# Performance work log

Measured on AMD Instinct MI355X. Metric: run time of the kernel, lower is better.

The kernel has to match this reference:

```python
import jax, jax.numpy as jnp
import numpy as np

N = 50000
E = 1600000
VOCAB = 1000
EMB = 128
HID = 128
OUT = 128


def setup_inputs() -> dict:
    key = jax.random.key(0)
    ks = jax.random.split(key, 8)
    labels = jax.random.randint(ks[0], (N,), 0, VOCAB)
    edge_index = jax.random.randint(ks[1], (2, E), 0, N)
    weight = jax.random.uniform(ks[2], (E,), dtype=jnp.float32)
    emb_table = jax.random.normal(ks[3], (VOCAB, EMB), dtype=jnp.float32) * 0.02
    W1 = jax.random.normal(ks[4], (EMB, HID), dtype=jnp.float32) * (1.0 / np.sqrt(EMB))
    b1 = jnp.zeros((HID,), dtype=jnp.float32)
    W2 = jax.random.normal(ks[5], (HID, OUT), dtype=jnp.float32) * (1.0 / np.sqrt(HID))
    b2 = jnp.zeros((OUT,), dtype=jnp.float32)
    return {"labels": labels, "edge_index": edge_index, "weight": weight,
            "emb_table": emb_table, "W1": W1, "b1": b1, "W2": W2, "b2": b2}


def _gcn_conv(x, src, dst, ew, W, b, n_nodes):
    # PyG GCNConv: linear transform, then symmetric-normalized weighted aggregation.
    x = x @ W  # [N, F_out]
    deg = jax.ops.segment_sum(ew, dst, num_segments=n_nodes)  # weighted in-degree (incl. self loops)
    dinv = jnp.where(deg > 0, jax.lax.rsqrt(deg), 0.0)
    norm = dinv[src] * ew * dinv[dst]  # [E_tot]
    msg = x[src] * norm[:, None]  # gather + scale
    out = jax.ops.segment_sum(msg, dst, num_segments=n_nodes)  # scatter-add
    return out + b


def reference(labels, edge_index, weight, emb_table, W1, b1, W2, b2):
    n_nodes = emb_table.shape[0] if False else labels.shape[0]
    # add self loops with weight 1.0 (GCNConv default add_self_loops=True)
    loop = jnp.arange(n_nodes, dtype=edge_index.dtype)
    src = jnp.concatenate([edge_index[0], loop])
    dst = jnp.concatenate([edge_index[1], loop])
    ew = jnp.concatenate([weight.astype(jnp.float32), jnp.ones((n_nodes,), jnp.float32)])

    x = emb_table[labels]  # embedding lookup [N, EMB]
    x = _gcn_conv(x, src, dst, ew, W1, b1, n_nodes)
    x = jax.nn.relu(x)
    x = _gcn_conv(x, src, dst, ew, W2, b2, n_nodes)
    return x
```

## Files before the change

kernel.cpp:

```cpp
#include <hip/hip_runtime.h>
#include <hip/hip_fp16.h>


#define CHUNKS 256
#define BSTAGE 2816

typedef float floatx2 __attribute__((ext_vector_type(2)));

__global__ __launch_bounds__(1024) void hist_temb_kernel(
    const int* __restrict__ dst, int* __restrict__ hist, int e, int chunk,
    int nb, int bact, const float* __restrict__ emb,
    const float* __restrict__ W1, __half* __restrict__ temb, int vocab) {
  __shared__ unsigned lh[1024];
  __shared__ float xs[8][128];
  int b = blockIdx.x, t = threadIdx.x;
  if (b < bact) {
    lh[t] = 0;
    __syncthreads();
    int start = b * chunk, end = min(e, start + chunk);
    for (int i = start + t; i < end; i += 1024) atomicAdd(&lh[dst[i] >> 6], 1u);
    __syncthreads();
    if (t < nb) hist[(size_t)t * CHUNKS + b] = (int)lh[t];
  } else {
    int r = (b - bact) * 8 + (t >> 7);
    int j = t & 127;
    if (r < vocab) xs[t >> 7][j] = emb[r * 128 + j];
    __syncthreads();
    if (r < vocab) {
      float acc = 0.f;
#pragma unroll 8
      for (int k = 0; k < 128; ++k) acc = fmaf(xs[t >> 7][k], W1[k * 128 + j], acc);
      temb[r * 128 + j] = __float2half_rn(acc);
    }
  }
}

__global__ __launch_bounds__(256) void colscan_kernel(const int* __restrict__ hist,
                                                      int* __restrict__ off,
                                                      int* __restrict__ tot,
                                                      int nb, int bact) {
  int k = (blockIdx.x * 256 + threadIdx.x) >> 6;
  int lane = threadIdx.x & 63;
  if (k >= nb) return;
  int carry = 0;
  for (int r = 0; r < CHUNKS / 64; ++r) {
    int b = r * 64 + lane;
    int h = (b < bact) ? hist[(size_t)k * CHUNKS + b] : 0;
    int x = h;
#pragma unroll
    for (int d = 1; d < 64; d <<= 1) {
      int tt = __shfl_up(x, d, 64);
      if (lane >= d) x += tt;
    }
    if (b < bact) off[(size_t)k * CHUNKS + b] = carry + x - h;
    carry += __shfl(x, 63, 64);
  }
  if (lane == 0) tot[k] = carry;
}

__global__ __launch_bounds__(1024) void ebase_kernel(const int* __restrict__ tot,
                                                     int* __restrict__ ebase, int nb) {
  __shared__ int wsum[16];
  int t = threadIdx.x, lane = t & 63, wv = t >> 6;
  int v = (t < nb) ? tot[t] : 0;
  int x = v;
#pragma unroll
  for (int d = 1; d < 64; d <<= 1) {
    int tt = __shfl_up(x, d, 64);
    if (lane >= d) x += tt;
  }
  if (lane == 63) wsum[wv] = x;
  __syncthreads();
  int o = 0;
#pragma unroll
  for (int w = 0; w < 16; ++w) o += (w < wv) ? wsum[w] : 0;
  int excl = x - v + o;
  if (t < nb) ebase[t] = excl;
  if (t == nb - 1) ebase[nb] = excl + v;
}

__global__ __launch_bounds__(1024) void scatter_kernel(
    const int* __restrict__ src, const int* __restrict__ dst,
    const float* __restrict__ w, const int* __restrict__ labels,
    const int* __restrict__ off, const int* __restrict__ ebase,
    int2* __restrict__ brec, int e, int chunk, int nb) {
  __shared__ unsigned bincnt[1024];
  __shared__ int gbase[1024];
  int b = blockIdx.x, t = threadIdx.x;
  bincnt[t] = 0;
  if (t < nb) gbase[t] = ebase[t] + off[(size_t)t * CHUNKS + b];
  __syncthreads();
  int start = b * chunk, end = min(e, start + chunk);
  int s[7], d[7], lb[7], ps[7];
  float wv[7];
#pragma unroll
  for (int u = 0; u < 7; ++u) {
    int i = start + u * 1024 + t;
    bool ok = i < end;
    s[u] = ok ? src[i] : 0;
    d[u] = ok ? dst[i] : 0;
    wv[u] = ok ? w[i] : 0.f;
  }
#pragma unroll
  for (int u = 0; u < 7; ++u) lb[u] = labels[s[u]];
#pragma unroll
  for (int u = 0; u < 7; ++u) ps[u] = gbase[d[u] >> 6];
#pragma unroll
  for (int u = 0; u < 7; ++u) {
    int i = start + u * 1024 + t;
    if (i < end) {
      int k = d[u] >> 6;
      unsigned lr = atomicAdd(&bincnt[k], 1u);
      unsigned rx = (unsigned)s[u] | ((unsigned)(d[u] & 63) << 16) |
                    ((unsigned)lb[u] << 22);
      brec[ps[u] + (int)lr] = make_int2((int)rx, __float_as_int(wv[u]));
    }
  }
}

__global__ __launch_bounds__(256) void bsort_kernel(const int2* __restrict__ brec,
                                                    const int* __restrict__ ebase,
                                                    int2* __restrict__ csr,
                                                    int* __restrict__ rs,
                                                    float* __restrict__ dinv, int n) {
  __shared__ int2 stage[BSTAGE];
  __shared__ unsigned h64[2][64];
  __shared__ unsigned cur[2][64];
  __shared__ float rsum[2][64];
  int k = blockIdx.x, t = threadIdx.x;
  int p = t >> 7;
  int e0 = ebase[k], e1 = ebase[k + 1], cnt = e1 - e0;
  if (t < 128) { h64[t >> 6][t & 63] = 0; rsum[t >> 6][t & 63] = 0.f; }
  __syncthreads();
  bool fits = (cnt <= BSTAGE);
  for (int i = t; i < cnt; i += 256) {
    int2 r = brec[e0 + i];
    if (fits) stage[i] = r;
    unsigned dl = ((unsigned)r.x >> 16) & 63u;
    atomicAdd(&h64[p][dl], 1u);
    atomicAdd(&rsum[p][dl], __int_as_float(r.y));
  }
  __syncthreads();
  if (t < 64) {
    int h0 = (int)h64[0][t];
    int hv = h0 + (int)h64[1][t];
    int x = hv;
#pragma unroll
    for (int d = 1; d < 64; d <<= 1) {
      int tt = __shfl_up(x, d, 64);
      if (t >= d) x += tt;
    }
    int ex = x - hv;
    cur[0][t] = (unsigned)(e0 + ex);
    cur[1][t] = (unsigned)(e0 + ex + h0);
    int v = k * 64 + t;
    if (v <= n) rs[v] = e0 + ex;
    if (v < n) dinv[v] = rsqrtf(1.0f + rsum[0][t] + rsum[1][t]);
  }
  __syncthreads();
  for (int i = t; i < cnt; i += 256) {
    int2 r = fits ? stage[i] : brec[e0 + i];
    unsigned rx = (unsigned)r.x;
    int dl = (int)((rx >> 16) & 63u);
    int pos = (int)atomicAdd(&cur[p][dl], 1u);
    csr[pos] = make_int2((int)((rx & 0xffffu) | ((rx >> 22) << 16)), r.y);
  }
}

__device__ __forceinline__ void unpack4(float2 raw, float2& a, float2& b) {
  union { float f; __half2 h; } u0, u1;
  u0.f = raw.x;
  u1.f = raw.y;
  a = __half22float2(u0.h);
  b = __half22float2(u1.h);
}

__global__ __launch_bounds__(256) void agg1_kernel(
    const int* __restrict__ rs, const int2* __restrict__ csr,
    const float* __restrict__ dinv, const int* __restrict__ labels,
    const __half* __restrict__ temb, const float* __restrict__ b1,
    unsigned* __restrict__ out8, int n) {
  int wid = (blockIdx.x * blockDim.x + threadIdx.x) >> 6;
  int lane = threadIdx.x & 63;
  if (wid >= n) return;
  int half = lane >> 5, fl = lane & 31;
  unsigned flo = (unsigned)(fl << 3);
  const char* tb = (const char*)temb;
  float di = dinv[wid];
  float acc0, acc1, acc2, acc3;
  {
    unsigned off = ((unsigned)labels[wid] << 8) + flo;
    float2 raw = *(const float2*)(tb + off);
    float2 a, b;
    unpack4(raw, a, b);
    float ss = half ? 0.f : di;
    acc0 = a.x * ss; acc1 = a.y * ss; acc2 = b.x * ss; acc3 = b.y * ss;
  }
  int base0 = rs[wid], r1v = rs[wid + 1];
  int s = 0;
  float v = 0.f;
  if (base0 + lane < r1v) {
    int2 c = csr[base0 + lane];
    s = c.x;
    v = __int_as_float(c.y) * dinv[c.x & 0xffff];
  }
  for (int base = base0; base < r1v; base += 64) {
    int ns = 0;
    float nv = 0.f;
    if (base + 64 + lane < r1v) {
      int2 c = csr[base + 64 + lane];
      ns = c.x;
      nv = __int_as_float(c.y) * dinv[c.x & 0xffff];
    }
    int nb = min(64, r1v - base);
    int j = 0;
    for (; j + 16 <= nb; j += 16) {
#pragma unroll
      for (int u = 0; u < 8; ++u) {
        int jj = j + 2 * u + half;
        int sj = __shfl(s, jj, 64);
        float vj = __shfl(v, jj, 64);
        unsigned off = (((unsigned)sj >> 16) << 8) + flo;
        float2 raw = *(const float2*)(tb + off);
        float2 a, b;
        unpack4(raw, a, b);
        acc0 = fmaf(a.x, vj, acc0); acc1 = fmaf(a.y, vj, acc1);
        acc2 = fmaf(b.x, vj, acc2); acc3 = fmaf(b.y, vj, acc3);
      }
    }
    for (; j + 2 <= nb; j += 2) {
      int jj = j + half;
      int sj = __shfl(s, jj, 64);
      float vj = __shfl(v, jj, 64);
      unsigned off = (((unsigned)sj >> 16) << 8) + flo;
      float2 raw = *(const float2*)(tb + off);
      float2 a, b;
      unpack4(raw, a, b);
      acc0 = fmaf(a.x, vj, acc0); acc1 = fmaf(a.y, vj, acc1);
      acc2 = fmaf(b.x, vj, acc2); acc3 = fmaf(b.y, vj, acc3);
    }
    if (j < nb) {
      int sj = __shfl(s, j, 64);
      float vj0 = __shfl(v, j, 64);
      float vj = half ? 0.f : vj0;
      unsigned off = (((unsigned)sj >> 16) << 8) + flo;
      float2 raw = *(const float2*)(tb + off);
      float2 a, b;
      unpack4(raw, a, b);
      acc0 = fmaf(a.x, vj, acc0); acc1 = fmaf(a.y, vj, acc1);
      acc2 = fmaf(b.x, vj, acc2); acc3 = fmaf(b.y, vj, acc3);
    }
    s = ns;
    v = nv;
  }
  acc0 += __shfl_xor(acc0, 32, 64);
  acc1 += __shfl_xor(acc1, 32, 64);
  acc2 += __shfl_xor(acc2, 32, 64);
  acc3 += __shfl_xor(acc3, 32, 64);
  if (half == 0) {
    float4 b4 = ((const float4*)b1)[fl];
    acc0 = fmaxf(fmaf(acc0, di, b4.x), 0.f) * 64.f;
    acc1 = fmaxf(fmaf(acc1, di, b4.y), 0.f) * 64.f;
    acc2 = fmaxf(fmaf(acc2, di, b4.z), 0.f) * 64.f;
    acc3 = fmaxf(fmaf(acc3, di, b4.w), 0.f) * 64.f;
    int pk = __builtin_amdgcn_cvt_pk_fp8_f32(acc0, acc1, 0, false);
    pk = __builtin_amdgcn_cvt_pk_fp8_f32(acc2, acc3, pk, true);
    out8[(size_t)wid * 32 + fl] = (unsigned)pk;
  }
}

__global__ __launch_bounds__(256) void agg2_kernel(
    const int* __restrict__ rs, const int2* __restrict__ csr,
    const float* __restrict__ dinv, const unsigned* __restrict__ h8,
    float* __restrict__ out, int n) {
  int wid = (blockIdx.x * blockDim.x + threadIdx.x) >> 6;
  int lane = threadIdx.x & 63;
  if (wid >= n) return;
  int half = lane >> 5, fl = lane & 31;
  unsigned flo = (unsigned)(fl << 2);
  const char* hb = (const char*)h8;
  float di = dinv[wid];
  float acc0, acc1, acc2, acc3;
  {
    unsigned r8 = *(const unsigned*)(hb + ((unsigned)wid << 7) + flo);
    floatx2 a = __builtin_amdgcn_cvt_pk_f32_fp8((int)r8, false);
    floatx2 b = __builtin_amdgcn_cvt_pk_f32_fp8((int)r8, true);
    float ss = half ? 0.f : di;
    acc0 = a[0] * ss; acc1 = a[1] * ss; acc2 = b[0] * ss; acc3 = b[1] * ss;
  }
  int base0 = rs[wid], r1v = rs[wid + 1];
  int s = 0;
  float v = 0.f;
  if (base0 + lane < r1v) {
    int2 c = csr[base0 + lane];
    s = c.x;
    v = __int_as_float(c.y) * dinv[c.x & 0xffff];
  }
  for (int base = base0; base < r1v; base += 64) {
    int ns = 0;
    float nv = 0.f;
    if (base + 64 + lane < r1v) {
      int2 c = csr[base + 64 + lane];
      ns = c.x;
      nv = __int_as_float(c.y) * dinv[c.x & 0xffff];
    }
    int nb = min(64, r1v - base);
    int j = 0;
    for (; j + 16 <= nb; j += 16) {
#pragma unroll
      for (int u = 0; u < 8; ++u) {
        int jj = j + 2 * u + half;
        int sj = __shfl(s, jj, 64);
        float vj = __shfl(v, jj, 64);
        unsigned off = (((unsigned)sj & 0xffffu) << 7) + flo;
        unsigned r8 = *(const unsigned*)(hb + off);
        floatx2 a = __builtin_amdgcn_cvt_pk_f32_fp8((int)r8, false);
        floatx2 b = __builtin_amdgcn_cvt_pk_f32_fp8((int)r8, true);
        acc0 = fmaf(a[0], vj, acc0); acc1 = fmaf(a[1], vj, acc1);
        acc2 = fmaf(b[0], vj, acc2); acc3 = fmaf(b[1], vj, acc3);
      }
    }
    for (; j + 2 <= nb; j += 2) {
      int jj = j + half;
      int sj = __shfl(s, jj, 64);
      float vj = __shfl(v, jj, 64);
      unsigned off = (((unsigned)sj & 0xffffu) << 7) + flo;
      unsigned r8 = *(const unsigned*)(hb + off);
      floatx2 a = __builtin_amdgcn_cvt_pk_f32_fp8((int)r8, false);
      floatx2 b = __builtin_amdgcn_cvt_pk_f32_fp8((int)r8, true);
      acc0 = fmaf(a[0], vj, acc0); acc1 = fmaf(a[1], vj, acc1);
      acc2 = fmaf(b[0], vj, acc2); acc3 = fmaf(b[1], vj, acc3);
    }
    if (j < nb) {
      int sj = __shfl(s, j, 64);
      float vj0 = __shfl(v, j, 64);
      float vj = half ? 0.f : vj0;
      unsigned off = (((unsigned)sj & 0xffffu) << 7) + flo;
      unsigned r8 = *(const unsigned*)(hb + off);
      floatx2 a = __builtin_amdgcn_cvt_pk_f32_fp8((int)r8, false);
      floatx2 b = __builtin_amdgcn_cvt_pk_f32_fp8((int)r8, true);
      acc0 = fmaf(a[0], vj, acc0); acc1 = fmaf(a[1], vj, acc1);
      acc2 = fmaf(b[0], vj, acc2); acc3 = fmaf(b[1], vj, acc3);
    }
    s = ns;
    v = nv;
  }
  acc0 += __shfl_xor(acc0, 32, 64);
  acc1 += __shfl_xor(acc1, 32, 64);
  acc2 += __shfl_xor(acc2, 32, 64);
  acc3 += __shfl_xor(acc3, 32, 64);
  if (half == 0) {
    float sc = di * 0.015625f;
    ((float4*)(out + (size_t)wid * 128))[fl] =
        make_float4(acc0 * sc, acc1 * sc, acc2 * sc, acc3 * sc);
  }
}

__global__ __launch_bounds__(256) void gemm_bias_kernel(float* __restrict__ y,
                                                        const float* __restrict__ W,
                                                        const float* __restrict__ bias,
                                                        int n) {
  __shared__ float xs[32][128];
  int tid = threadIdx.x;
  int tc = tid & 31;
  int tr = tid >> 5;
  int rb = blockIdx.x * 32;
  {
    const float4* xg = (const float4*)(y + (size_t)rb * 128);
    float4* xls = (float4*)&xs[0][0];
#pragma unroll
    for (int i = 0; i < 4; ++i) {
      int idx = tid + i * 256;
      int row = rb + (idx >> 5);
      float4 val = (row < n) ? xg[idx] : make_float4(0.f, 0.f, 0.f, 0.f);
      xls[idx] = val;
    }
  }
  __syncthreads();
  int j0 = tc * 4;
  float4 b4 = *(const float4*)(bias + j0);
  float acc[4][4];
#pragma unroll
  for (int r = 0; r < 4; ++r) {
    acc[r][0] = b4.x; acc[r][1] = b4.y; acc[r][2] = b4.z; acc[r][3] = b4.w;
  }
#pragma unroll 4
  for (int k = 0; k < 128; ++k) {
    float4 w4 = *(const float4*)(W + k * 128 + j0);
#pragma unroll
    for (int r = 0; r < 4; ++r) {
      float xv = xs[tr * 4 + r][k];
      acc[r][0] = fmaf(xv, w4.x, acc[r][0]);
      acc[r][1] = fmaf(xv, w4.y, acc[r][1]);
      acc[r][2] = fmaf(xv, w4.z, acc[r][2]);
      acc[r][3] = fmaf(xv, w4.w, acc[r][3]);
    }
  }
#pragma unroll
  for (int r = 0; r < 4; ++r) {
    int row = rb + tr * 4 + r;
    if (row < n)
      *(float4*)(y + (size_t)row * 128 + j0) =
          make_float4(acc[r][0], acc[r][1], acc[r][2], acc[r][3]);
  }
}

extern "C" void kernel_launch(void* const* d_in, const int* in_sizes, int n_in,
                              void* d_out, int out_size, void* d_ws, size_t ws_size,
                              hipStream_t stream) {
  const int* labels = (const int*)d_in[0];
  const int* edge_index = (const int*)d_in[1];
  const float* weight = (const float*)d_in[2];
  const float* emb = (const float*)d_in[3];
  const float* W1 = (const float*)d_in[4];
  const float* b1 = (const float*)d_in[5];
  const float* W2 = (const float*)d_in[6];
  const float* b2 = (const float*)d_in[7];

  int n = in_sizes[0];
  int e = in_sizes[1] / 2;
  int vocab = in_sizes[3] / 128;
  const int* srcp = edge_index;
  const int* dstp = edge_index + e;

  int nb = (n + 63) >> 6;
  int chunk = (e + CHUNKS - 1) / CHUNKS;
  int bact = (e + chunk - 1) / chunk;
  int tblocks = (vocab + 7) / 8;

  float* ws = (float*)d_ws;
  size_t o = 0;
  auto alloc_f = [&](size_t c) { float* p = ws + o; o += (c + 255) & ~(size_t)255; return p; };
  int*      hist  = (int*)alloc_f((size_t)nb * CHUNKS);
  int*      off   = (int*)alloc_f((size_t)nb * CHUNKS);
  int*      tot   = (int*)alloc_f(nb);
  int*      ebase = (int*)alloc_f(nb + 1);
  int2*     brec  = (int2*)alloc_f((size_t)e * 2);
  int*      rs    = (int*)alloc_f(n + 1);
  int2*     csr   = (int2*)alloc_f((size_t)e * 2);
  float*    dinv  = alloc_f(n);
  __half*   temb  = (__half*)alloc_f((size_t)vocab * 64);
  unsigned* out8  = (unsigned*)alloc_f((size_t)n * 32);
  (void)ws_size;

  dim3 b256(256);
  dim3 b1024(1024);
  int gagg = (int)(((size_t)n * 64 + 255) / 256);

  hist_temb_kernel<<<bact + tblocks, b1024, 0, stream>>>(dstp, hist, e, chunk, nb,
                                                         bact, emb, W1, temb, vocab);
  colscan_kernel<<<(nb * 64 + 255) / 256, b256, 0, stream>>>(hist, off, tot, nb, bact);
  ebase_kernel<<<1, b1024, 0, stream>>>(tot, ebase, nb);
  scatter_kernel<<<bact, b1024, 0, stream>>>(srcp, dstp, weight, labels, off, ebase,
                                             brec, e, chunk, nb);
  bsort_kernel<<<nb, b256, 0, stream>>>(brec, ebase, csr, rs, dinv, n);
  agg1_kernel<<<gagg, b256, 0, stream>>>(rs, csr, dinv, labels, temb, b1, out8, n);
  agg2_kernel<<<gagg, b256, 0, stream>>>(rs, csr, dinv, out8, (float*)d_out, n);
  gemm_bias_kernel<<<(n + 31) / 32, b256, 0, stream>>>((float*)d_out, W2, b2, n);
}
```

Baseline: 165.6 us.

## Repack CSR to 4-byte records with prescaled fp16 weights and store temb in fp8

Adds a repack kernel that turns each 8-byte CSR record into two 4-byte arrays, one per aggregation pass. Each packs the needed source index (label or node id) with an fp16 edge weight already multiplied by dinv[src]. The aggregation kernels therefore no longer do a per-edge dinv gather, and the streamed edge data is halved. The embedding-times-W1 table is now stored in fp8 scaled by 64 instead of fp16, which shrinks gathered rows, and that GEMM uses float4 loads with 32 rows per block. The cost is an extra kernel pass over all edges and lower precision in both the edge weights and the first-layer features.

```diff
diff --git a/kernel.cpp b/kernel.cpp
--- a/kernel.cpp
+++ b/kernel.cpp
@@ -10,9 +10,9 @@
 __global__ __launch_bounds__(1024) void hist_temb_kernel(
     const int* __restrict__ dst, int* __restrict__ hist, int e, int chunk,
     int nb, int bact, const float* __restrict__ emb,
-    const float* __restrict__ W1, __half* __restrict__ temb, int vocab) {
+    const float* __restrict__ W1, unsigned* __restrict__ temb8, int vocab) {
   __shared__ unsigned lh[1024];
-  __shared__ float xs[8][128];
+  __shared__ float xs[32][128];
   int b = blockIdx.x, t = threadIdx.x;
   if (b < bact) {
     lh[t] = 0;
@@ -22,15 +22,23 @@
     __syncthreads();
     if (t < nb) hist[(size_t)t * CHUNKS + b] = (int)lh[t];
   } else {
-    int r = (b - bact) * 8 + (t >> 7);
-    int j = t & 127;
-    if (r < vocab) xs[t >> 7][j] = emb[r * 128 + j];
+    int row = t >> 5, fl = t & 31;
+    int r = (b - bact) * 32 + row;
+    if (r < vocab)
+      *(float4*)&xs[row][fl * 4] = *(const float4*)(emb + (size_t)r * 128 + fl * 4);
     __syncthreads();
     if (r < vocab) {
-      float acc = 0.f;
-#pragma unroll 8
-      for (int k = 0; k < 128; ++k) acc = fmaf(xs[t >> 7][k], W1[k * 128 + j], acc);
-      temb[r * 128 + j] = __float2half_rn(acc);
+      float a0 = 0.f, a1 = 0.f, a2 = 0.f, a3 = 0.f;
+#pragma unroll 4
+      for (int k = 0; k < 128; ++k) {
+        float xv = xs[row][k];
+        float4 w4 = *(const float4*)(W1 + k * 128 + fl * 4);
+        a0 = fmaf(xv, w4.x, a0); a1 = fmaf(xv, w4.y, a1);
+        a2 = fmaf(xv, w4.z, a2); a3 = fmaf(xv, w4.w, a3);
+      }
+      int pk = __builtin_amdgcn_cvt_pk_fp8_f32(a0 * 64.f, a1 * 64.f, 0, false);
+      pk = __builtin_amdgcn_cvt_pk_fp8_f32(a2 * 64.f, a3 * 64.f, pk, true);
+      temb8[(size_t)r * 32 + fl] = (unsigned)pk;
     }
   }
 }
@@ -167,91 +175,93 @@
   }
 }
 
-__device__ __forceinline__ void unpack4(float2 raw, float2& a, float2& b) {
-  union { float f; __half2 h; } u0, u1;
-  u0.f = raw.x;
-  u1.f = raw.y;
-  a = __half22float2(u0.h);
-  b = __half22float2(u1.h);
+__global__ __launch_bounds__(256) void repack_kernel(const int2* __restrict__ csr,
+                                                     const float* __restrict__ dinv,
+                                                     unsigned* __restrict__ csrA,
+                                                     unsigned* __restrict__ csrB,
+                                                     int e) {
+  int i = blockIdx.x * 1024 + threadIdx.x;
+  int2 c[4];
+  float wp[4];
+#pragma unroll
+  for (int u = 0; u < 4; ++u) {
+    int k = i + u * 256;
+    c[u] = (k < e) ? csr[k] : make_int2(0, 0);
+  }
+#pragma unroll
+  for (int u = 0; u < 4; ++u)
+    wp[u] = __int_as_float(c[u].y) * dinv[c[u].x & 0xffff];
+#pragma unroll
+  for (int u = 0; u < 4; ++u) {
+    int k = i + u * 256;
+    if (k < e) {
+      unsigned hb = (unsigned)__half_as_ushort(__float2half_rn(wp[u]));
+      csrA[k] = ((((unsigned)c[u].x) >> 16) << 16) | hb;
+      csrB[k] = (((unsigned)c[u].x) << 16) | hb;
+    }
+  }
 }
 
 __global__ __launch_bounds__(256) void agg1_kernel(
-    const int* __restrict__ rs, const int2* __restrict__ csr,
+    const int* __restrict__ rs, const unsigned* __restrict__ csrA,
     const float* __restrict__ dinv, const int* __restrict__ labels,
-    const __half* __restrict__ temb, const float* __restrict__ b1,
+    const unsigned* __restrict__ temb8, const float* __restrict__ b1,
     unsigned* __restrict__ out8, int n) {
   int wid = (blockIdx.x * blockDim.x + threadIdx.x) >> 6;
   int lane = threadIdx.x & 63;
   if (wid >= n) return;
   int half = lane >> 5, fl = lane & 31;
-  unsigned flo = (unsigned)(fl << 3);
-  const char* tb = (const char*)temb;
+  unsigned flo = (unsigned)(fl << 2);
+  const char* tb = (const char*)temb8;
   float di = dinv[wid];
   float acc0, acc1, acc2, acc3;
   {
-    unsigned off = ((unsigned)labels[wid] << 8) + flo;
-    float2 raw = *(const float2*)(tb + off);
-    float2 a, b;
-    unpack4(raw, a, b);
+    unsigned r8 = *(const unsigned*)(tb + (((unsigned)labels[wid]) << 7) + flo);
+    floatx2 a = __builtin_amdgcn_cvt_pk_f32_fp8((int)r8, false);
+    floatx2 b = __builtin_amdgcn_cvt_pk_f32_fp8((int)r8, true);
     float ss = half ? 0.f : di;
-    acc0 = a.x * ss; acc1 = a.y * ss; acc2 = b.x * ss; acc3 = b.y * ss;
+    acc0 = a[0] * ss; acc1 = a[1] * ss; acc2 = b[0] * ss; acc3 = b[1] * ss;
   }
   int base0 = rs[wid], r1v = rs[wid + 1];
-  int s = 0;
-  float v = 0.f;
-  if (base0 + lane < r1v) {
-    int2 c = csr[base0 + lane];
-    s = c.x;
-    v = __int_as_float(c.y) * dinv[c.x & 0xffff];
-  }
+  unsigned x = 0;
+  if (base0 + lane < r1v) x = csrA[base0 + lane];
   for (int base = base0; base < r1v; base += 64) {
-    int ns = 0;
-    float nv = 0.f;
-    if (base + 64 + lane < r1v) {
-      int2 c = csr[base + 64 + lane];
-      ns = c.x;
-      nv = __int_as_float(c.y) * dinv[c.x & 0xffff];
-    }
+    unsigned nx = 0;
+    if (base + 64 + lane < r1v) nx = csrA[base + 64 + lane];
     int nb = min(64, r1v - base);
     int j = 0;
     for (; j + 16 <= nb; j += 16) {
 #pragma unroll
       for (int u = 0; u < 8; ++u) {
-        int jj = j + 2 * u + half;
-        int sj = __shfl(s, jj, 64);
-        float vj = __shfl(v, jj, 64);
-        unsigned off = (((unsigned)sj >> 16) << 8) + flo;
-        float2 raw = *(const float2*)(tb + off);
-        float2 a, b;
-        unpack4(raw, a, b);
-        acc0 = fmaf(a.x, vj, acc0); acc1 = fmaf(a.y, vj, acc1);
-        acc2 = fmaf(b.x, vj, acc2); acc3 = fmaf(b.y, vj, acc3);
+        unsigned xj = (unsigned)__shfl((int)x, j + 2 * u + half, 64);
+        float vj = __half2float(__ushort_as_half((unsigned short)(xj & 0xffffu)));
+        unsigned r8 = *(const unsigned*)(tb + ((xj >> 16) << 7) + flo);
+        floatx2 a = __builtin_amdgcn_cvt_pk_f32_fp8((int)r8, false);
+        floatx2 b = __builtin_amdgcn_cvt_pk_f32_fp8((int)r8, true);
+        acc0 = fmaf(a[0], vj, acc0); acc1 = fmaf(a[1], vj, acc1);
+        acc2 = fmaf(b[0], vj, acc2); acc3 = fmaf(b[1], vj, acc3);
       }
     }
     for (; j + 2 <= nb; j += 2) {
-      int jj = j + half;
-      int sj = __shfl(s, jj, 64);
-      float vj = __shfl(v, jj, 64);
-      unsigned off = (((unsigned)sj >> 16) << 8) + flo;
-      float2 raw = *(const float2*)(tb + off);
-      float2 a, b;
-      unpack4(raw, a, b);
-      acc0 = fmaf(a.x, vj, acc0); acc1 = fmaf(a.y, vj, acc1);
-      acc2 = fmaf(b.x, vj, acc2); acc3 = fmaf(b.y, vj, acc3);
+      unsigned xj = (unsigned)__shfl((int)x, j + half, 64);
+      float vj = __half2float(__ushort_as_half((unsigned short)(xj & 0xffffu)));
+      unsigned r8 = *(const unsigned*)(tb + ((xj >> 16) << 7) + flo);
+      floatx2 a = __builtin_amdgcn_cvt_pk_f32_fp8((int)r8, false);
+      floatx2 b = __builtin_amdgcn_cvt_pk_f32_fp8((int)r8, true);
+      acc0 = fmaf(a[0], vj, acc0); acc1 = fmaf(a[1], vj, acc1);
+      acc2 = fmaf(b[0], vj, acc2); acc3 = fmaf(b[1], vj, acc3);
     }
     if (j < nb) {
-      int sj = __shfl(s, j, 64);
-      float vj0 = __shfl(v, j, 64);
+      unsigned xj = (unsigned)__shfl((int)x, j, 64);
+      float vj0 = __half2float(__ushort_as_half((unsigned short)(xj & 0xffffu)));
       float vj = half ? 0.f : vj0;
-      unsigned off = (((unsigned)sj >> 16) << 8) + flo;
-      float2 raw = *(const float2*)(tb + off);
-      float2 a, b;
-      unpack4(raw, a, b);
-      acc0 = fmaf(a.x, vj, acc0); acc1 = fmaf(a.y, vj, acc1);
-      acc2 = fmaf(b.x, vj, acc2); acc3 = fmaf(b.y, vj, acc3);
-    }
-    s = ns;
-    v = nv;
+      unsigned r8 = *(const unsigned*)(tb + ((xj >> 16) << 7) + flo);
+      floatx2 a = __builtin_amdgcn_cvt_pk_f32_fp8((int)r8, false);
+      floatx2 b = __builtin_amdgcn_cvt_pk_f32_fp8((int)r8, true);
+      acc0 = fmaf(a[0], vj, acc0); acc1 = fmaf(a[1], vj, acc1);
+      acc2 = fmaf(b[0], vj, acc2); acc3 = fmaf(b[1], vj, acc3);
+    }
+    x = nx;
   }
   acc0 += __shfl_xor(acc0, 32, 64);
   acc1 += __shfl_xor(acc1, 32, 64);
@@ -259,10 +269,10 @@
   acc3 += __shfl_xor(acc3, 32, 64);
   if (half == 0) {
     float4 b4 = ((const float4*)b1)[fl];
-    acc0 = fmaxf(fmaf(acc0, di, b4.x), 0.f) * 64.f;
-    acc1 = fmaxf(fmaf(acc1, di, b4.y), 0.f) * 64.f;
-    acc2 = fmaxf(fmaf(acc2, di, b4.z), 0.f) * 64.f;
-    acc3 = fmaxf(fmaf(acc3, di, b4.w), 0.f) * 64.f;
+    acc0 = fmaxf(fmaf(acc0, di, b4.x * 64.f), 0.f);
+    acc1 = fmaxf(fmaf(acc1, di, b4.y * 64.f), 0.f);
+    acc2 = fmaxf(fmaf(acc2, di, b4.z * 64.f), 0.f);
+    acc3 = fmaxf(fmaf(acc3, di, b4.w * 64.f), 0.f);
     int pk = __builtin_amdgcn_cvt_pk_fp8_f32(acc0, acc1, 0, false);
     pk = __builtin_amdgcn_cvt_pk_fp8_f32(acc2, acc3, pk, true);
     out8[(size_t)wid * 32 + fl] = (unsigned)pk;
@@ -270,7 +280,7 @@
 }
 
 __global__ __launch_bounds__(256) void agg2_kernel(
-    const int* __restrict__ rs, const int2* __restrict__ csr,
+    const int* __restrict__ rs, const unsigned* __restrict__ csrB,
     const float* __restrict__ dinv, const unsigned* __restrict__ h8,
     float* __restrict__ out, int n) {
   int wid = (blockIdx.x * blockDim.x + threadIdx.x) >> 6;
@@ -282,38 +292,26 @@
   float di = dinv[wid];
   float acc0, acc1, acc2, acc3;
   {
-    unsigned r8 = *(const unsigned*)(hb + ((unsigned)wid << 7) + flo);
+    unsigned r8 = *(const unsigned*)(hb + (((unsigned)wid) << 7) + flo);
     floatx2 a = __builtin_amdgcn_cvt_pk_f32_fp8((int)r8, false);
     floatx2 b = __builtin_amdgcn_cvt_pk_f32_fp8((int)r8, true);
     float ss = half ? 0.f : di;
     acc0 = a[0] * ss; acc1 = a[1] * ss; acc2 = b[0] * ss; acc3 = b[1] * ss;
   }
   int base0 = rs[wid], r1v = rs[wid + 1];
-  int s = 0;
-  float v = 0.f;
-  if (base0 + lane < r1v) {
-    int2 c = csr[base0 + lane];
-    s = c.x;
-    v = __int_as_float(c.y) * dinv[c.x & 0xffff];
-  }
+  unsigned x = 0;
+  if (base0 + lane < r1v) x = csrB[base0 + lane];
   for (int base = base0; base < r1v; base += 64) {
-    int ns = 0;
-    float nv = 0.f;
-    if (base + 64 + lane < r1v) {
-      int2 c = csr[base + 64 + lane];
-      ns = c.x;
-      nv = __int_as_float(c.y) * dinv[c.x & 0xffff];
-    }
+    unsigned nx = 0;
+    if (base + 64 + lane < r1v) nx = csrB[base + 64 + lane];
     int nb = min(64, r1v - base);
     int j = 0;
     for (; j + 16 <= nb; j += 16) {
 #pragma unroll
       for (int u = 0; u < 8; ++u) {
-        int jj = j + 2 * u + half;
-        int sj = __shfl(s, jj, 64);
-        float vj = __shfl(v, jj, 64);
-        unsigned off = (((unsigned)sj & 0xffffu) << 7) + flo;
-        unsigned r8 = *(const unsigned*)(hb + off);
+        unsigned xj = (unsigned)__shfl((int)x, j + 2 * u + half, 64);
+        float vj = __half2float(__ushort_as_half((unsigned short)(xj & 0xffffu)));
+        unsigned r8 = *(const unsigned*)(hb + ((xj >> 16) << 7) + flo);
         floatx2 a = __builtin_amdgcn_cvt_pk_f32_fp8((int)r8, false);
         floatx2 b = __builtin_amdgcn_cvt_pk_f32_fp8((int)r8, true);
         acc0 = fmaf(a[0], vj, acc0); acc1 = fmaf(a[1], vj, acc1);
@@ -321,29 +319,25 @@
       }
     }
     for (; j + 2 <= nb; j += 2) {
-      int jj = j + half;
-      int sj = __shfl(s, jj, 64);
-      float vj = __shfl(v, jj, 64);
-      unsigned off = (((unsigned)sj & 0xffffu) << 7) + flo;
-      unsigned r8 = *(const unsigned*)(hb + off);
+      unsigned xj = (unsigned)__shfl((int)x, j + half, 64);
+      float vj = __half2float(__ushort_as_half((unsigned short)(xj & 0xffffu)));
+      unsigned r8 = *(const unsigned*)(hb + ((xj >> 16) << 7) + flo);
       floatx2 a = __builtin_amdgcn_cvt_pk_f32_fp8((int)r8, false);
       floatx2 b = __builtin_amdgcn_cvt_pk_f32_fp8((int)r8, true);
       acc0 = fmaf(a[0], vj, acc0); acc1 = fmaf(a[1], vj, acc1);
       acc2 = fmaf(b[0], vj, acc2); acc3 = fmaf(b[1], vj, acc3);
     }
     if (j < nb) {
-      int sj = __shfl(s, j, 64);
-      float vj0 = __shfl(v, j, 64);
+      unsigned xj = (unsigned)__shfl((int)x, j, 64);
+      float vj0 = __half2float(__ushort_as_half((unsigned short)(xj & 0xffffu)));
       float vj = half ? 0.f : vj0;
-      unsigned off = (((unsigned)sj & 0xffffu) << 7) + flo;
-      unsigned r8 = *(const unsigned*)(hb + off);
+      unsigned r8 = *(const unsigned*)(hb + ((xj >> 16) << 7) + flo);
       floatx2 a = __builtin_amdgcn_cvt_pk_f32_fp8((int)r8, false);
       floatx2 b = __builtin_amdgcn_cvt_pk_f32_fp8((int)r8, true);
       acc0 = fmaf(a[0], vj, acc0); acc1 = fmaf(a[1], vj, acc1);
       acc2 = fmaf(b[0], vj, acc2); acc3 = fmaf(b[1], vj, acc3);
     }
-    s = ns;
-    v = nv;
+    x = nx;
   }
   acc0 += __shfl_xor(acc0, 32, 64);
   acc1 += __shfl_xor(acc1, 32, 64);
@@ -426,7 +420,7 @@
   int nb = (n + 63) >> 6;
   int chunk = (e + CHUNKS - 1) / CHUNKS;
   int bact = (e + chunk - 1) / chunk;
-  int tblocks = (vocab + 7) / 8;
+  int tblocks = (vocab + 31) / 32;
 
   float* ws = (float*)d_ws;
   size_t o = 0;
@@ -438,8 +432,10 @@
   int2*     brec  = (int2*)alloc_f((size_t)e * 2);
   int*      rs    = (int*)alloc_f(n + 1);
   int2*     csr   = (int2*)alloc_f((size_t)e * 2);
+  unsigned* csrA  = (unsigned*)alloc_f(e);
+  unsigned* csrB  = (unsigned*)alloc_f(e);
   float*    dinv  = alloc_f(n);
-  __half*   temb  = (__half*)alloc_f((size_t)vocab * 64);
+  unsigned* temb8 = (unsigned*)alloc_f((size_t)vocab * 32);
   unsigned* out8  = (unsigned*)alloc_f((size_t)n * 32);
   (void)ws_size;
 
@@ -448,13 +444,14 @@
   int gagg = (int)(((size_t)n * 64 + 255) / 256);
 
   hist_temb_kernel<<<bact + tblocks, b1024, 0, stream>>>(dstp, hist, e, chunk, nb,
-                                                         bact, emb, W1, temb, vocab);
+                                                         bact, emb, W1, temb8, vocab);
   colscan_kernel<<<(nb * 64 + 255) / 256, b256, 0, stream>>>(hist, off, tot, nb, bact);
   ebase_kernel<<<1, b1024, 0, stream>>>(tot, ebase, nb);
   scatter_kernel<<<bact, b1024, 0, stream>>>(srcp, dstp, weight, labels, off, ebase,
                                              brec, e, chunk, nb);
   bsort_kernel<<<nb, b256, 0, stream>>>(brec, ebase, csr, rs, dinv, n);
-  agg1_kernel<<<gagg, b256, 0, stream>>>(rs, csr, dinv, labels, temb, b1, out8, n);
-  agg2_kernel<<<gagg, b256, 0, stream>>>(rs, csr, dinv, out8, (float*)d_out, n);
+  repack_kernel<<<(e + 1023) / 1024, b256, 0, stream>>>(csr, dinv, csrA, csrB, e);
+  agg1_kernel<<<gagg, b256, 0, stream>>>(rs, csrA, dinv, labels, temb8, b1, out8, n);
+  agg2_kernel<<<gagg, b256, 0, stream>>>(rs, csrB, dinv, out8, (float*)d_out, n);
   gemm_bias_kernel<<<(n + 31) / 32, b256, 0, stream>>>((float*)d_out, W2, b2, n);
 }
```

Result: no change. 167.5 us (+1.1%).

## Process two destination nodes per wavefront in both aggregation kernels

Applied to the files above, without the earlier changes.

Each wavefront now aggregates two destination rows at once, interleaving their CSR prefetches and gathers so more independent memory loads are in flight per wave. The grid is halved to match. The inner loop is regrouped into batches of 8 edges, with loads for A and B issued before their FMAs. This costs more registers and lanes sit idle when the two nodes have unequal degree. The epilogue writes A from the lower half and B from the upper half.

```diff
diff --git a/kernel.cpp b/kernel.cpp
--- a/kernel.cpp
+++ b/kernel.cpp
@@ -180,92 +180,129 @@
     const float* __restrict__ dinv, const int* __restrict__ labels,
     const __half* __restrict__ temb, const float* __restrict__ b1,
     unsigned* __restrict__ out8, int n) {
-  int wid = (blockIdx.x * blockDim.x + threadIdx.x) >> 6;
+  int gw = (blockIdx.x * blockDim.x + threadIdx.x) >> 6;
+  int widA = gw * 2;
+  if (widA >= n) return;
+  int widB = widA + 1;
+  bool hasB = widB < n;
   int lane = threadIdx.x & 63;
-  if (wid >= n) return;
   int half = lane >> 5, fl = lane & 31;
   unsigned flo = (unsigned)(fl << 3);
   const char* tb = (const char*)temb;
-  float di = dinv[wid];
-  float acc0, acc1, acc2, acc3;
+  float diA = dinv[widA];
+  float diB = hasB ? dinv[widB] : 0.f;
+  float aA0, aA1, aA2, aA3;
+  float aB0 = 0.f, aB1 = 0.f, aB2 = 0.f, aB3 = 0.f;
   {
-    unsigned off = ((unsigned)labels[wid] << 8) + flo;
-    float2 raw = *(const float2*)(tb + off);
+    float2 raw = *(const float2*)(tb + ((unsigned)labels[widA] << 8) + flo);
     float2 a, b;
     unpack4(raw, a, b);
-    float ss = half ? 0.f : di;
-    acc0 = a.x * ss; acc1 = a.y * ss; acc2 = b.x * ss; acc3 = b.y * ss;
-  }
-  int base0 = rs[wid], r1v = rs[wid + 1];
-  int s = 0;
-  float v = 0.f;
-  if (base0 + lane < r1v) {
-    int2 c = csr[base0 + lane];
-    s = c.x;
-    v = __int_as_float(c.y) * dinv[c.x & 0xffff];
-  }
-  for (int base = base0; base < r1v; base += 64) {
-    int ns = 0;
-    float nv = 0.f;
-    if (base + 64 + lane < r1v) {
-      int2 c = csr[base + 64 + lane];
-      ns = c.x;
-      nv = __int_as_float(c.y) * dinv[c.x & 0xffff];
-    }
-    int nb = min(64, r1v - base);
-    int j = 0;
-    for (; j + 16 <= nb; j += 16) {
-#pragma unroll
-      for (int u = 0; u < 8; ++u) {
-        int jj = j + 2 * u + half;
-        int sj = __shfl(s, jj, 64);
-        float vj = __shfl(v, jj, 64);
-        unsigned off = (((unsigned)sj >> 16) << 8) + flo;
-        float2 raw = *(const float2*)(tb + off);
-        float2 a, b;
-        unpack4(raw, a, b);
-        acc0 = fmaf(a.x, vj, acc0); acc1 = fmaf(a.y, vj, acc1);
-        acc2 = fmaf(b.x, vj, acc2); acc3 = fmaf(b.y, vj, acc3);
-      }
-    }
-    for (; j + 2 <= nb; j += 2) {
-      int jj = j + half;
-      int sj = __shfl(s, jj, 64);
-      float vj = __shfl(v, jj, 64);
-      unsigned off = (((unsigned)sj >> 16) << 8) + flo;
-      float2 raw = *(const float2*)(tb + off);
-      float2 a, b;
-      unpack4(raw, a, b);
-      acc0 = fmaf(a.x, vj, acc0); acc1 = fmaf(a.y, vj, acc1);
-      acc2 = fmaf(b.x, vj, acc2); acc3 = fmaf(b.y, vj, acc3);
-    }
-    if (j < nb) {
-      int sj = __shfl(s, j, 64);
-      float vj0 = __shfl(v, j, 64);
-      float vj = half ? 0.f : vj0;
-      unsigned off = (((unsigned)sj >> 16) << 8) + flo;
-      float2 raw = *(const float2*)(tb + off);
-      float2 a, b;
-      unpack4(raw, a, b);
-      acc0 = fmaf(a.x, vj, acc0); acc1 = fmaf(a.y, vj, acc1);
-      acc2 = fmaf(b.x, vj, acc2); acc3 = fmaf(b.y, vj, acc3);
-    }
-    s = ns;
-    v = nv;
-  }
-  acc0 += __shfl_xor(acc0, 32, 64);
-  acc1 += __shfl_xor(acc1, 32, 64);
-  acc2 += __shfl_xor(acc2, 32, 64);
-  acc3 += __shfl_xor(acc3, 32, 64);
+    float ss = half ? 0.f : diA;
+    aA0 = a.x * ss; aA1 = a.y * ss; aA2 = b.x * ss; aA3 = b.y * ss;
+  }
+  if (hasB) {
+    float2 raw = *(const float2*)(tb + ((unsigned)labels[widB] << 8) + flo);
+    float2 a, b;
+    unpack4(raw, a, b);
+    float ss = half ? diB : 0.f;
+    aB0 = a.x * ss; aB1 = a.y * ss; aB2 = b.x * ss; aB3 = b.y * ss;
+  }
+  int baseA = rs[widA], r1A = rs[widA + 1];
+  int baseB = hasB ? rs[widB] : 0, r1B = hasB ? rs[widB + 1] : 0;
+  int sA = 0, sB = 0;
+  float vA = 0.f, vB = 0.f;
+  if (baseA + lane < r1A) {
+    int2 c = csr[baseA + lane];
+    sA = c.x;
+    vA = __int_as_float(c.y) * dinv[c.x & 0xffff];
+  }
+  if (baseB + lane < r1B) {
+    int2 c = csr[baseB + lane];
+    sB = c.x;
+    vB = __int_as_float(c.y) * dinv[c.x & 0xffff];
+  }
+  while (baseA < r1A || baseB < r1B) {
+    int nsA = 0, nsB = 0;
+    float nvA = 0.f, nvB = 0.f;
+    if (baseA + 64 + lane < r1A) {
+      int2 c = csr[baseA + 64 + lane];
+      nsA = c.x;
+      nvA = __int_as_float(c.y) * dinv[c.x & 0xffff];
+    }
+    if (baseB + 64 + lane < r1B) {
+      int2 c = csr[baseB + 64 + lane];
+      nsB = c.x;
+      nvB = __int_as_float(c.y) * dinv[c.x & 0xffff];
+    }
+    int nbA = min(64, max(0, r1A - baseA));
+    int nbB = min(64, max(0, r1B - baseB));
+    int nbmax = max(nbA, nbB);
+    for (int j = 0; j < nbmax; j += 8) {
+      bool doA = j < nbA, doB = j < nbB;
+      float2 rA[4], rB[4];
+      float wjA[4], wjB[4];
+      if (doA) {
+#pragma unroll
+        for (int u = 0; u < 4; ++u) {
+          int jj = j + 2 * u + half;
+          int sj = __shfl(sA, jj, 64);
+          wjA[u] = __shfl(vA, jj, 64);
+          rA[u] = *(const float2*)(tb + ((((unsigned)sj) >> 16) << 8) + flo);
+        }
+      }
+      if (doB) {
+#pragma unroll
+        for (int u = 0; u < 4; ++u) {
+          int jj = j + 2 * u + half;
+          int sj = __shfl(sB, jj, 64);
+          wjB[u] = __shfl(vB, jj, 64);
+          rB[u] = *(const float2*)(tb + ((((unsigned)sj) >> 16) << 8) + flo);
+        }
+      }
+      if (doA) {
+#pragma unroll
+        for (int u = 0; u < 4; ++u) {
+          float2 a, b;
+          unpack4(rA[u], a, b);
+          aA0 = fmaf(a.x, wjA[u], aA0); aA1 = fmaf(a.y, wjA[u], aA1);
+          aA2 = fmaf(b.x, wjA[u], aA2); aA3 = fmaf(b.y, wjA[u], aA3);
+        }
+      }
+      if (doB) {
+#pragma unroll
+        for (int u = 0; u < 4; ++u) {
+          float2 a, b;
+          unpack4(rB[u], a, b);
+          aB0 = fmaf(a.x, wjB[u], aB0); aB1 = fmaf(a.y, wjB[u], aB1);
+          aB2 = fmaf(b.x, wjB[u], aB2); aB3 = fmaf(b.y, wjB[u], aB3);
+        }
+      }
+    }
+    baseA += 64;
+    baseB += 64;
+    sA = nsA; vA = nvA; sB = nsB; vB = nvB;
+  }
+  aA0 += __shfl_xor(aA0, 32, 64); aA1 += __shfl_xor(aA1, 32, 64);
+  aA2 += __shfl_xor(aA2, 32, 64); aA3 += __shfl_xor(aA3, 32, 64);
+  aB0 += __shfl_xor(aB0, 32, 64); aB1 += __shfl_xor(aB1, 32, 64);
+  aB2 += __shfl_xor(aB2, 32, 64); aB3 += __shfl_xor(aB3, 32, 64);
+  float4 b4 = ((const float4*)b1)[fl];
   if (half == 0) {
-    float4 b4 = ((const float4*)b1)[fl];
-    acc0 = fmaxf(fmaf(acc0, di, b4.x), 0.f) * 64.f;
-    acc1 = fmaxf(fmaf(acc1, di, b4.y), 0.f) * 64.f;
-    acc2 = fmaxf(fmaf(acc2, di, b4.z), 0.f) * 64.f;
-    acc3 = fmaxf(fmaf(acc3, di, b4.w), 0.f) * 64.f;
-    int pk = __builtin_amdgcn_cvt_pk_fp8_f32(acc0, acc1, 0, false);
-    pk = __builtin_amdgcn_cvt_pk_fp8_f32(acc2, acc3, pk, true);
-    out8[(size_t)wid * 32 + fl] = (unsigned)pk;
+    float o0 = fmaxf(fmaf(aA0, diA, b4.x), 0.f) * 64.f;
+    float o1 = fmaxf(fmaf(aA1, diA, b4.y), 0.f) * 64.f;
+    float o2 = fmaxf(fmaf(aA2, diA, b4.z), 0.f) * 64.f;
+    float o3 = fmaxf(fmaf(aA3, diA, b4.w), 0.f) * 64.f;
+    int pk = __builtin_amdgcn_cvt_pk_fp8_f32(o0, o1, 0, false);
+    pk = __builtin_amdgcn_cvt_pk_fp8_f32(o2, o3, pk, true);
+    out8[(size_t)widA * 32 + fl] = (unsigned)pk;
+  } else if (hasB) {
+    float o0 = fmaxf(fmaf(aB0, diB, b4.x), 0.f) * 64.f;
+    float o1 = fmaxf(fmaf(aB1, diB, b4.y), 0.f) * 64.f;
+    float o2 = fmaxf(fmaf(aB2, diB, b4.z), 0.f) * 64.f;
+    float o3 = fmaxf(fmaf(aB3, diB, b4.w), 0.f) * 64.f;
+    int pk = __builtin_amdgcn_cvt_pk_fp8_f32(o0, o1, 0, false);
+    pk = __builtin_amdgcn_cvt_pk_fp8_f32(o2, o3, pk, true);
+    out8[(size_t)widB * 32 + fl] = (unsigned)pk;
   }
 }
 
@@ -273,86 +310,120 @@
     const int* __restrict__ rs, const int2* __restrict__ csr,
     const float* __restrict__ dinv, const unsigned* __restrict__ h8,
     float* __restrict__ out, int n) {
-  int wid = (blockIdx.x * blockDim.x + threadIdx.x) >> 6;
+  int gw = (blockIdx.x * blockDim.x + threadIdx.x) >> 6;
+  int widA = gw * 2;
+  if (widA >= n) return;
+  int widB = widA + 1;
+  bool hasB = widB < n;
   int lane = threadIdx.x & 63;
-  if (wid >= n) return;
   int half = lane >> 5, fl = lane & 31;
   unsigned flo = (unsigned)(fl << 2);
   const char* hb = (const char*)h8;
-  float di = dinv[wid];
-  float acc0, acc1, acc2, acc3;
+  float diA = dinv[widA];
+  float diB = hasB ? dinv[widB] : 0.f;
+  float aA0, aA1, aA2, aA3;
+  float aB0 = 0.f, aB1 = 0.f, aB2 = 0.f, aB3 = 0.f;
   {
-    unsigned r8 = *(const unsigned*)(hb + ((unsigned)wid << 7) + flo);
+    unsigned r8 = *(const unsigned*)(hb + ((unsigned)widA << 7) + flo);
     floatx2 a = __builtin_amdgcn_cvt_pk_f32_fp8((int)r8, false);
     floatx2 b = __builtin_amdgcn_cvt_pk_f32_fp8((int)r8, true);
-    float ss = half ? 0.f : di;
-    acc0 = a[0] * ss; acc1 = a[1] * ss; acc2 = b[0] * ss; acc3 = b[1] * ss;
-  }
-  int base0 = rs[wid], r1v = rs[wid + 1];
-  int s = 0;
-  float v = 0.f;
-  if (base0 + lane < r1v) {
-    int2 c = csr[base0 + lane];
-    s = c.x;
-    v = __int_as_float(c.y) * dinv[c.x & 0xffff];
-  }
-  for (int base = base0; base < r1v; base += 64) {
-    int ns = 0;
-    float nv = 0.f;
-    if (base + 64 + lane < r1v) {
-      int2 c = csr[base + 64 + lane];
-      ns = c.x;
-      nv = __int_as_float(c.y) * dinv[c.x & 0xffff];
-    }
-    int nb = min(64, r1v - base);
-    int j = 0;
-    for (; j + 16 <= nb; j += 16) {
-#pragma unroll
-      for (int u = 0; u < 8; ++u) {
-        int jj = j + 2 * u + half;
-        int sj = __shfl(s, jj, 64);
-        float vj = __shfl(v, jj, 64);
-        unsigned off = (((unsigned)sj & 0xffffu) << 7) + flo;
-        unsigned r8 = *(const unsigned*)(hb + off);
-        floatx2 a = __builtin_amdgcn_cvt_pk_f32_fp8((int)r8, false);
-        floatx2 b = __builtin_amdgcn_cvt_pk_f32_fp8((int)r8, true);
-        acc0 = fmaf(a[0], vj, acc0); acc1 = fmaf(a[1], vj, acc1);
-        acc2 = fmaf(b[0], vj, acc2); acc3 = fmaf(b[1], vj, acc3);
-      }
-    }
-    for (; j + 2 <= nb; j += 2) {
-      int jj = j + half;
-      int sj = __shfl(s, jj, 64);
-      float vj = __shfl(v, jj, 64);
-      unsigned off = (((unsigned)sj & 0xffffu) << 7) + flo;
-      unsigned r8 = *(const unsigned*)(hb + off);
-      floatx2 a = __builtin_amdgcn_cvt_pk_f32_fp8((int)r8, false);
-      floatx2 b = __builtin_amdgcn_cvt_pk_f32_fp8((int)r8, true);
-      acc0 = fmaf(a[0], vj, acc0); acc1 = fmaf(a[1], vj, acc1);
-      acc2 = fmaf(b[0], vj, acc2); acc3 = fmaf(b[1], vj, acc3);
-    }
-    if (j < nb) {
-      int sj = __shfl(s, j, 64);
-      float vj0 = __shfl(v, j, 64);
-      float vj = half ? 0.f : vj0;
-      unsigned off = (((unsigned)sj & 0xffffu) << 7) + flo;
-      unsigned r8 = *(const unsigned*)(hb + off);
-      floatx2 a = __builtin_amdgcn_cvt_pk_f32_fp8((int)r8, false);
-      floatx2 b = __builtin_amdgcn_cvt_pk_f32_fp8((int)r8, true);
-      acc0 = fmaf(a[0], vj, acc0); acc1 = fmaf(a[1], vj, acc1);
-      acc2 = fmaf(b[0], vj, acc2); acc3 = fmaf(b[1], vj, acc3);
-    }
-    s = ns;
-    v = nv;
-  }
-  acc0 += __shfl_xor(acc0, 32, 64);
-  acc1 += __shfl_xor(acc1, 32, 64);
-  acc2 += __shfl_xor(acc2, 32, 64);
-  acc3 += __shfl_xor(acc3, 32, 64);
+    float ss = half ? 0.f : diA;
+    aA0 = a[0] * ss; aA1 = a[1] * ss; aA2 = b[0] * ss; aA3 = b[1] * ss;
+  }
+  if (hasB) {
+    unsigned r8 = *(const unsigned*)(hb + ((unsigned)widB << 7) + flo);
+    floatx2 a = __builtin_amdgcn_cvt_pk_f32_fp8((int)r8, false);
+    floatx2 b = __builtin_amdgcn_cvt_pk_f32_fp8((int)r8, true);
+    float ss = half ? diB : 0.f;
+    aB0 = a[0] * ss; aB1 = a[1] * ss; aB2 = b[0] * ss; aB3 = b[1] * ss;
+  }
+  int baseA = rs[widA], r1A = rs[widA + 1];
+  int baseB = hasB ? rs[widB] : 0, r1B = hasB ? rs[widB + 1] : 0;
+  int sA = 0, sB = 0;
+  float vA = 0.f, vB = 0.f;
+  if (baseA + lane < r1A) {
+    int2 c = csr[baseA + lane];
+    sA = c.x;
+    vA = __int_as_float(c.y) * dinv[c.x & 0xffff];
+  }
+  if (baseB + lane < r1B) {
+    int2 c = csr[baseB + lane];
+    sB = c.x;
+    vB = __int_as_float(c.y) * dinv[c.x & 0xffff];
+  }
+  while (baseA < r1A || baseB < r1B) {
+    int nsA = 0, nsB = 0;
+    float nvA = 0.f, nvB = 0.f;
+    if (baseA + 64 + lane < r1A) {
+      int2 c = csr[baseA + 64 + lane];
+      nsA = c.x;
+      nvA = __int_as_float(c.y) * dinv[c.x & 0xffff];
+    }
+    if (baseB + 64 + lane < r1B) {
+      int2 c = csr[baseB + 64 + lane];
+      nsB = c.x;
+      nvB = __int_as_float(c.y) * dinv[c.x & 0xffff];
+    }
+    int nbA = min(64, max(0, r1A - baseA));
+    int nbB = min(64, max(0, r1B - baseB));
+    int nbmax = max(nbA, nbB);
+    for (int j = 0; j < nbmax; j += 8) {
+      bool doA = j < nbA, doB = j < nbB;
+      unsigned rA[4], rB[4];
+      float wjA[4], wjB[4];
+      if (doA) {
+#pragma unroll
+        for (int u = 0; u < 4; ++u) {
+          int jj = j + 2 * u + half;
+          int sj = __shfl(sA, jj, 64);
+          wjA[u] = __shfl(vA, jj, 64);
+          rA[u] = *(const unsigned*)(hb + ((((unsigned)sj) & 0xffffu) << 7) + flo);
+        }
+      }
+      if (doB) {
+#pragma unroll
+        for (int u = 0; u < 4; ++u) {
+          int jj = j + 2 * u + half;
+          int sj = __shfl(sB, jj, 64);
+          wjB[u] = __shfl(vB, jj, 64);
+          rB[u] = *(const unsigned*)(hb + ((((unsigned)sj) & 0xffffu) << 7) + flo);
+        }
+      }
+      if (doA) {
+#pragma unroll
+        for (int u = 0; u < 4; ++u) {
+          floatx2 a = __builtin_amdgcn_cvt_pk_f32_fp8((int)rA[u], false);
+          floatx2 b = __builtin_amdgcn_cvt_pk_f32_fp8((int)rA[u], true);
+          aA0 = fmaf(a[0], wjA[u], aA0); aA1 = fmaf(a[1], wjA[u], aA1);
+          aA2 = fmaf(b[0], wjA[u], aA2); aA3 = fmaf(b[1], wjA[u], aA3);
+        }
+      }
+      if (doB) {
+#pragma unroll
+        for (int u = 0; u < 4; ++u) {
+          floatx2 a = __builtin_amdgcn_cvt_pk_f32_fp8((int)rB[u], false);
+          floatx2 b = __builtin_amdgcn_cvt_pk_f32_fp8((int)rB[u], true);
+          aB0 = fmaf(a[0], wjB[u], aB0); aB1 = fmaf(a[1], wjB[u], aB1);
+          aB2 = fmaf(b[0], wjB[u], aB2); aB3 = fmaf(b[1], wjB[u], aB3);
+        }
+      }
+    }
+    baseA += 64;
+    baseB += 64;
+    sA = nsA; vA = nvA; sB = nsB; vB = nvB;
+  }
+  aA0 += __shfl_xor(aA0, 32, 64); aA1 += __shfl_xor(aA1, 32, 64);
+  aA2 += __shfl_xor(aA2, 32, 64); aA3 += __shfl_xor(aA3, 32, 64);
+  aB0 += __shfl_xor(aB0, 32, 64); aB1 += __shfl_xor(aB1, 32, 64);
+  aB2 += __shfl_xor(aB2, 32, 64); aB3 += __shfl_xor(aB3, 32, 64);
   if (half == 0) {
-    float sc = di * 0.015625f;
-    ((float4*)(out + (size_t)wid * 128))[fl] =
-        make_float4(acc0 * sc, acc1 * sc, acc2 * sc, acc3 * sc);
+    float sc = diA * 0.015625f;
+    ((float4*)(out + (size_t)widA * 128))[fl] =
+        make_float4(aA0 * sc, aA1 * sc, aA2 * sc, aA3 * sc);
+  } else if (hasB) {
+    float sc = diB * 0.015625f;
+    ((float4*)(out + (size_t)widB * 128))[fl] =
+        make_float4(aB0 * sc, aB1 * sc, aB2 * sc, aB3 * sc);
   }
 }
 
@@ -445,7 +516,8 @@
 
   dim3 b256(256);
   dim3 b1024(1024);
-  int gagg = (int)(((size_t)n * 64 + 255) / 256);
+  int nwaves = (n + 1) / 2;
+  int gagg = (int)(((size_t)nwaves * 64 + 255) / 256);
 
   hist_temb_kernel<<<bact + tblocks, b1024, 0, stream>>>(dstp, hist, e, chunk, nb,
                                                          bact, emb, W1, temb, vocab);
```

Result: no change. 165.2 us (-0.3%).
